# Kernel tuning notes

Hardware: AMD Instinct MI355X
Metric: run time of the kernel (lower is better)

Reference implementation:

```python
import jax, jax.numpy as jnp
import numpy as np

FP8_MAX = 448.0  # max finite value of float8_e4m3fn


def quantize_tensorwise(x):
    """Tensorwise fp8 quantization: returns fp8 tensor and inverse scale."""
    amax = jnp.max(jnp.abs(x))
    inv_scale = jnp.maximum(amax, jnp.asarray(1e-12, x.dtype)) / FP8_MAX
    q = (x / inv_scale).astype(jnp.float8_e4m3fn)
    return q, inv_scale


def setup_inputs() -> dict:
    key = jax.random.key(0)
    k1, k2, k3 = jax.random.split(key, 3)
    x = jax.random.normal(k1, (4, 1024, 4096), dtype=jnp.float32)
    weight = jax.random.normal(k2, (4096, 4096), dtype=jnp.float32) * 0.02
    bias = jax.random.normal(k3, (4096,), dtype=jnp.float32)
    return {"x": x, "weight": weight, "bias": bias}


def reference(x, weight, bias):
    out_shape = (*x.shape[:-1], weight.shape[0])
    xm = x.reshape(-1, x.shape[-1])                    # [M, K]
    fp8_x, x_inv_scale = quantize_tensorwise(xm)       # fp8 input + tensorwise scale
    fp8_wt, w_inv_scale = quantize_tensorwise(weight.T)  # weight.t() quantized, [K, N]
    # fp8 GEMM with inline dequant: (fp8_x @ fp8_w.T) * sx * sw + bias
    acc = jnp.matmul(fp8_x.astype(jnp.float32), fp8_wt.astype(jnp.float32))
    out = acc * (x_inv_scale * w_inv_scale) + bias.astype(jnp.float32)
    return out.reshape(out_shape).astype(x.dtype)
```

## Files before the change

### kernel.cpp

```cpp
#include <hip/hip_runtime.h>
#include <hip/hip_bf16.h>
#include <stdint.h>

static constexpr int M = 4096, N = 4096, K = 4096;
static constexpr float FP8_MAX = 448.0f;

using f32x16 = __attribute__((ext_vector_type(16))) float;
using i32x4  = __attribute__((ext_vector_type(4))) int;
using i32x8  = __attribute__((ext_vector_type(8))) int;

static constexpr size_t AQ_OFF   = 0;
static constexpr size_t BQ_OFF   = (size_t)M * K;
static constexpr size_t AMAX_OFF = BQ_OFF + (size_t)N * K;

__global__ __launch_bounds__(256) void amax_kernel(const float* __restrict__ x,
                                                   const float* __restrict__ w,
                                                   float* __restrict__ amax,
                                                   int n4_per_tensor,
                                                   int blocks_per_tensor) {
    const int tensor = blockIdx.x / blocks_per_tensor;
    const int blk    = blockIdx.x % blocks_per_tensor;
    const float4* src = (const float4*)(tensor == 0 ? x : w);

    float m = 0.0f;
    for (int i = blk * blockDim.x + threadIdx.x; i < n4_per_tensor;
         i += blocks_per_tensor * blockDim.x) {
        float4 v = src[i];
        m = fmaxf(m, fmaxf(fmaxf(fabsf(v.x), fabsf(v.y)),
                           fmaxf(fabsf(v.z), fabsf(v.w))));
    }
    #pragma unroll
    for (int off = 32; off >= 1; off >>= 1)
        m = fmaxf(m, __shfl_xor(m, off, 64));

    __shared__ float sm[4];
    const int lane = threadIdx.x & 63, wid = threadIdx.x >> 6;
    if (lane == 0) sm[wid] = m;
    __syncthreads();
    if (threadIdx.x == 0) {
        m = fmaxf(fmaxf(sm[0], sm[1]), fmaxf(sm[2], sm[3]));
        atomicMax((unsigned int*)&amax[tensor], __float_as_uint(m));
    }
}

__global__ __launch_bounds__(256) void quant_kernel(const float* __restrict__ x,
                                                    const float* __restrict__ w,
                                                    unsigned char* __restrict__ aq,
                                                    unsigned char* __restrict__ bq,
                                                    const float* __restrict__ amax,
                                                    int n4_per_tensor) {
    int gid = blockIdx.x * blockDim.x + threadIdx.x;
    const int tensor = (gid >= n4_per_tensor) ? 1 : 0;
    const int i = tensor ? gid - n4_per_tensor : gid;

    const float inv = fmaxf(amax[tensor], 1e-12f) / FP8_MAX;
    const float4* src = (const float4*)(tensor == 0 ? x : w);

    float4 v = src[i];
    float q0 = v.x / inv, q1 = v.y / inv, q2 = v.z / inv, q3 = v.w / inv;
    int packed = __builtin_amdgcn_cvt_pk_fp8_f32(q0, q1, 0, false);
    packed     = __builtin_amdgcn_cvt_pk_fp8_f32(q2, q3, packed, true);

    if (tensor == 0) {
        ((int*)aq)[i] = packed;
    } else {
        const int n  = i >> 10;
        const int k0 = (i & 1023) * 4;
        const int blk = (n >> 5) * (K / 64) + (k0 >> 6);
        const int ln  = (n & 31) + 32 * ((k0 >> 5) & 1);
        ((int*)bq)[blk * 512 + ln * 8 + ((k0 >> 2) & 7)] = packed;
    }
}

static constexpr int BM = 256, BN = 256, BK = 64, DEPTH = 4, NT = K / BK;

__device__ __forceinline__ void gld_lds16(const void* g, void* l) {
    __builtin_amdgcn_global_load_lds(
        (const __attribute__((address_space(1))) void*)g,
        (__attribute__((address_space(3))) void*)l, 16, 0, 0);
}

struct BReg { i32x4 lo0, hi0, lo1, hi1; };

__global__ __launch_bounds__(512, 2) void gemm_kernel(const unsigned char* __restrict__ Aq,
                                                      const unsigned char* __restrict__ Bq,
                                                      const float* __restrict__ amax,
                                                      const float* __restrict__ bias,
                                                      float* __restrict__ out) {
    __shared__ unsigned char lds[DEPTH][BM * BK];

    const int tid  = threadIdx.x;
    const int lane = tid & 63;
    const int w    = tid >> 6;
    const int wr   = w >> 2, wc = w & 3;

    const int bid = blockIdx.x;
    const int swz = (bid & 7) * 32 + (bid >> 3);
    const int brow = (swz >> 4) * BM;
    const int bcol = (swz & 15) * BN;

    const float sx = fmaxf(amax[0], 1e-12f) / FP8_MAX;
    const float sw = fmaxf(amax[1], 1e-12f) / FP8_MAX;
    const float scale = sx * sw;

    const int r4    = lane >> 2;
    const int row0  = w * 16 + r4;
    const int chk   = ((lane & 3) ^ ((row0 >> 1) & 3)) * 16;
    const unsigned char* Abase = Aq + (size_t)brow * K;

    const int frow = lane & 31;
    const int swzr = (frow >> 1) & 3;
    const int c0   = (lane >> 5) * 2;
    const int off0 = ((c0 ^ swzr) << 4);
    const int off1 = (((c0 + 1) ^ swzr) << 4);

    const unsigned char* Bf0 =
        Bq + (size_t)((bcol >> 5) + wc * 2 + 0) * (K / 64) * 2048 + (size_t)lane * 32;
    const unsigned char* Bf1 =
        Bq + (size_t)((bcol >> 5) + wc * 2 + 1) * (K / 64) * 2048 + (size_t)lane * 32;

    f32x16 acc[4][2] = {};

#define STAGE_A(t, d)                                                                          \
    do {                                                                                       \
        const size_t _k0 = (size_t)(t) * BK;                                                   \
        gld_lds16(Abase + (size_t)row0 * K + _k0 + chk,         &lds[d][w * 1024]);            \
        gld_lds16(Abase + (size_t)(row0 + 128) * K + _k0 + chk, &lds[d][8192 + w * 1024]);     \
    } while (0)

#define GLOAD_B(t, BR)                                                         \
    do {                                                                       \
        const size_t _o = (size_t)(t) * 2048;                                  \
        BR.lo0 = *(const i32x4*)(Bf0 + _o);                                    \
        BR.hi0 = *(const i32x4*)(Bf0 + _o + 16);                               \
        BR.lo1 = *(const i32x4*)(Bf1 + _o);                                    \
        BR.hi1 = *(const i32x4*)(Bf1 + _o + 16);                               \
    } while (0)

#define ITER(t, rs, ss, BRcur, BRld)                                           \
    do {                                                                       \
        asm volatile("s_waitcnt vmcnt(12)" ::: "memory");                      \
        __builtin_amdgcn_s_barrier();                                          \
        __builtin_amdgcn_sched_barrier(0);                                     \
        STAGE_A(((t) + 3 < NT) ? (t) + 3 : NT - 1, ss);                        \
        GLOAD_B(((t) + 2 < NT) ? (t) + 2 : NT - 1, BRld);                      \
        i32x8 _aF[4];                                                          \
        _Pragma("unroll")                                                      \
        for (int _mt = 0; _mt < 4; ++_mt) {                                    \
            const unsigned char* _p = &lds[rs][(wr * 128 + _mt * 32 + frow) * BK]; \
            i32x4 _lo = *(const i32x4*)(_p + off0);                            \
            i32x4 _hi = *(const i32x4*)(_p + off1);                            \
            _aF[_mt] = __builtin_shufflevector(_lo, _hi, 0, 1, 2, 3, 4, 5, 6, 7); \
        }                                                                      \
        i32x8 _b0 = __builtin_shufflevector(BRcur.lo0, BRcur.hi0, 0, 1, 2, 3, 4, 5, 6, 7); \
        i32x8 _b1 = __builtin_shufflevector(BRcur.lo1, BRcur.hi1, 0, 1, 2, 3, 4, 5, 6, 7); \
        __builtin_amdgcn_s_setprio(1);                                         \
        _Pragma("unroll")                                                      \
        for (int _mt = 0; _mt < 4; ++_mt) {                                    \
            acc[_mt][0] = __builtin_amdgcn_mfma_scale_f32_32x32x64_f8f6f4(     \
                _aF[_mt], _b0, acc[_mt][0], 0, 0, 0, 0x7F, 0, 0x7F);           \
            acc[_mt][1] = __builtin_amdgcn_mfma_scale_f32_32x32x64_f8f6f4(     \
                _aF[_mt], _b1, acc[_mt][1], 0, 0, 0, 0x7F, 0, 0x7F);           \
        }                                                                      \
        __builtin_amdgcn_s_setprio(0);                                         \
        asm volatile("s_waitcnt lgkmcnt(0)" ::: "memory");                     \
        __builtin_amdgcn_sched_barrier(0);                                     \
    } while (0)

    BReg br0, br1, br2, br3;

    STAGE_A(0, 0);
    GLOAD_B(0, br0);
    STAGE_A(1, 1);
    GLOAD_B(1, br1);
    STAGE_A(2, 2);
    asm volatile("s_waitcnt vmcnt(0)" ::: "memory");
    __builtin_amdgcn_s_barrier();
    __builtin_amdgcn_sched_barrier(0);

    for (int t = 0; t < NT; t += 4) {
        ITER(t + 0, 0, 3, br0, br2);
        ITER(t + 1, 1, 0, br1, br3);
        ITER(t + 2, 2, 1, br2, br0);
        ITER(t + 3, 3, 2, br3, br1);
    }
#undef ITER
#undef GLOAD_B
#undef STAGE_A

    #pragma unroll
    for (int mt = 0; mt < 4; ++mt) {
        const int rbase = brow + wr * 128 + mt * 32 + 4 * (lane >> 5);
        #pragma unroll
        for (int nt2 = 0; nt2 < 2; ++nt2) {
            const int col = bcol + wc * 64 + nt2 * 32 + (lane & 31);
            const float b = bias[col];
            #pragma unroll
            for (int reg = 0; reg < 16; ++reg) {
                const int row = rbase + (reg & 3) + 8 * (reg >> 2);
                out[(size_t)row * N + col] = acc[mt][nt2][reg] * scale + b;
            }
        }
    }
}

extern "C" void kernel_launch(void* const* d_in, const int* in_sizes, int n_in,
                              void* d_out, int out_size, void* d_ws, size_t ws_size,
                              hipStream_t stream) {
    const float* x    = (const float*)d_in[0];
    const float* w    = (const float*)d_in[1];
    const float* bias = (const float*)d_in[2];
    float* out = (float*)d_out;

    unsigned char* aq = (unsigned char*)d_ws + AQ_OFF;
    unsigned char* bq = (unsigned char*)d_ws + BQ_OFF;
    float* amax = (float*)((unsigned char*)d_ws + AMAX_OFF);

    const int n4 = (M * K) / 4;

    hipMemsetAsync(amax, 0, 2 * sizeof(float), stream);

    const int blocks_per_tensor = 512;
    amax_kernel<<<2 * blocks_per_tensor, 256, 0, stream>>>(x, w, amax, n4, blocks_per_tensor);

    const int quant_blocks = (2 * n4) / 256;
    quant_kernel<<<quant_blocks, 256, 0, stream>>>(x, w, aq, bq, amax, n4);

    gemm_kernel<<<256, 512, 0, stream>>>(aq, bq, amax, bias, out);
}
```

Before: 138.2 us.

## Halve GEMM M-tile to 128 and restructure B prefetch to double-buffer

```diff
diff --git a/kernel.cpp b/kernel.cpp
--- a/kernel.cpp
+++ b/kernel.cpp
@@ -72,7 +72,7 @@
     }
 }
 
-static constexpr int BM = 256, BN = 256, BK = 64, DEPTH = 4, NT = K / BK;
+static constexpr int BM = 128, BN = 256, BK = 64, DEPTH = 4, NT = K / BK;
 
 __device__ __forceinline__ void gld_lds16(const void* g, void* l) {
     __builtin_amdgcn_global_load_lds(
@@ -80,9 +80,9 @@
         (__attribute__((address_space(3))) void*)l, 16, 0, 0);
 }
 
-struct BReg { i32x4 lo0, hi0, lo1, hi1; };
-
-__global__ __launch_bounds__(512, 2) void gemm_kernel(const unsigned char* __restrict__ Aq,
+struct BPair { i32x8 b0, b1; };
+
+__global__ __launch_bounds__(512, 4) void gemm_kernel(const unsigned char* __restrict__ Aq,
                                                       const unsigned char* __restrict__ Bq,
                                                       const float* __restrict__ amax,
                                                       const float* __restrict__ bias,
@@ -95,7 +95,7 @@
     const int wr   = w >> 2, wc = w & 3;
 
     const int bid = blockIdx.x;
-    const int swz = (bid & 7) * 32 + (bid >> 3);
+    const int swz = (bid & 7) * 64 + (bid >> 3);
     const int brow = (swz >> 4) * BM;
     const int bcol = (swz & 15) * BN;
 
@@ -103,9 +103,8 @@
     const float sw = fmaxf(amax[1], 1e-12f) / FP8_MAX;
     const float scale = sx * sw;
 
-    const int r4    = lane >> 2;
-    const int row0  = w * 16 + r4;
-    const int chk   = ((lane & 3) ^ ((row0 >> 1) & 3)) * 16;
+    const int row0  = tid >> 2;
+    const int chk   = ((tid & 3) ^ ((row0 >> 1) & 3)) * 16;
     const unsigned char* Abase = Aq + (size_t)brow * K;
 
     const int frow = lane & 31;
@@ -119,78 +118,76 @@
     const unsigned char* Bf1 =
         Bq + (size_t)((bcol >> 5) + wc * 2 + 1) * (K / 64) * 2048 + (size_t)lane * 32;
 
-    f32x16 acc[4][2] = {};
-
-#define STAGE_A(t, d)                                                                          \
-    do {                                                                                       \
-        const size_t _k0 = (size_t)(t) * BK;                                                   \
-        gld_lds16(Abase + (size_t)row0 * K + _k0 + chk,         &lds[d][w * 1024]);            \
-        gld_lds16(Abase + (size_t)(row0 + 128) * K + _k0 + chk, &lds[d][8192 + w * 1024]);     \
-    } while (0)
+    f32x16 acc[2][2] = {};
+
+#define STAGE_A(t, d)                                                          \
+    gld_lds16(Abase + (size_t)row0 * K + (size_t)(t) * BK + chk,               \
+              &lds[d][(tid >> 6) * 1024])
 
 #define GLOAD_B(t, BR)                                                         \
     do {                                                                       \
         const size_t _o = (size_t)(t) * 2048;                                  \
-        BR.lo0 = *(const i32x4*)(Bf0 + _o);                                    \
-        BR.hi0 = *(const i32x4*)(Bf0 + _o + 16);                               \
-        BR.lo1 = *(const i32x4*)(Bf1 + _o);                                    \
-        BR.hi1 = *(const i32x4*)(Bf1 + _o + 16);                               \
+        BR.b0 = *(const i32x8*)(Bf0 + _o);                                     \
+        BR.b1 = *(const i32x8*)(Bf1 + _o);                                     \
     } while (0)
 
-#define ITER(t, rs, ss, BRcur, BRld)                                           \
+#define ITER(t, rs, ss, BCUR, BNXT)                                            \
     do {                                                                       \
-        asm volatile("s_waitcnt vmcnt(12)" ::: "memory");                      \
+        asm volatile("s_waitcnt vmcnt(1)" ::: "memory");                       \
         __builtin_amdgcn_s_barrier();                                          \
         __builtin_amdgcn_sched_barrier(0);                                     \
+        GLOAD_B(((t) + 1 < NT) ? (t) + 1 : NT - 1, BNXT);                      \
         STAGE_A(((t) + 3 < NT) ? (t) + 3 : NT - 1, ss);                        \
-        GLOAD_B(((t) + 2 < NT) ? (t) + 2 : NT - 1, BRld);                      \
-        i32x8 _aF[4];                                                          \
-        _Pragma("unroll")                                                      \
-        for (int _mt = 0; _mt < 4; ++_mt) {                                    \
-            const unsigned char* _p = &lds[rs][(wr * 128 + _mt * 32 + frow) * BK]; \
+        i32x8 _a0, _a1;                                                        \
+        {                                                                      \
+            const unsigned char* _p = &lds[rs][(wr * 64 + frow) * BK];         \
             i32x4 _lo = *(const i32x4*)(_p + off0);                            \
             i32x4 _hi = *(const i32x4*)(_p + off1);                            \
-            _aF[_mt] = __builtin_shufflevector(_lo, _hi, 0, 1, 2, 3, 4, 5, 6, 7); \
+            _a0 = __builtin_shufflevector(_lo, _hi, 0, 1, 2, 3, 4, 5, 6, 7);   \
         }                                                                      \
-        i32x8 _b0 = __builtin_shufflevector(BRcur.lo0, BRcur.hi0, 0, 1, 2, 3, 4, 5, 6, 7); \
-        i32x8 _b1 = __builtin_shufflevector(BRcur.lo1, BRcur.hi1, 0, 1, 2, 3, 4, 5, 6, 7); \
+        {                                                                      \
+            const unsigned char* _p = &lds[rs][(wr * 64 + 32 + frow) * BK];    \
+            i32x4 _lo = *(const i32x4*)(_p + off0);                            \
+            i32x4 _hi = *(const i32x4*)(_p + off1);                            \
+            _a1 = __builtin_shufflevector(_lo, _hi, 0, 1, 2, 3, 4, 5, 6, 7);   \
+        }                                                                      \
         __builtin_amdgcn_s_setprio(1);                                         \
-        _Pragma("unroll")                                                      \
-        for (int _mt = 0; _mt < 4; ++_mt) {                                    \
-            acc[_mt][0] = __builtin_amdgcn_mfma_scale_f32_32x32x64_f8f6f4(     \
-                _aF[_mt], _b0, acc[_mt][0], 0, 0, 0, 0x7F, 0, 0x7F);           \
-            acc[_mt][1] = __builtin_amdgcn_mfma_scale_f32_32x32x64_f8f6f4(     \
-                _aF[_mt], _b1, acc[_mt][1], 0, 0, 0, 0x7F, 0, 0x7F);           \
-        }                                                                      \
+        acc[0][0] = __builtin_amdgcn_mfma_scale_f32_32x32x64_f8f6f4(           \
+            _a0, BCUR.b0, acc[0][0], 0, 0, 0, 0x7F, 0, 0x7F);                  \
+        acc[0][1] = __builtin_amdgcn_mfma_scale_f32_32x32x64_f8f6f4(           \
+            _a0, BCUR.b1, acc[0][1], 0, 0, 0, 0x7F, 0, 0x7F);                  \
+        acc[1][0] = __builtin_amdgcn_mfma_scale_f32_32x32x64_f8f6f4(           \
+            _a1, BCUR.b0, acc[1][0], 0, 0, 0, 0x7F, 0, 0x7F);                  \
+        acc[1][1] = __builtin_amdgcn_mfma_scale_f32_32x32x64_f8f6f4(           \
+            _a1, BCUR.b1, acc[1][1], 0, 0, 0, 0x7F, 0, 0x7F);                  \
         __builtin_amdgcn_s_setprio(0);                                         \
         asm volatile("s_waitcnt lgkmcnt(0)" ::: "memory");                     \
         __builtin_amdgcn_sched_barrier(0);                                     \
     } while (0)
 
-    BReg br0, br1, br2, br3;
+    BPair bP, bQ;
 
     STAGE_A(0, 0);
-    GLOAD_B(0, br0);
     STAGE_A(1, 1);
-    GLOAD_B(1, br1);
     STAGE_A(2, 2);
+    GLOAD_B(0, bP);
     asm volatile("s_waitcnt vmcnt(0)" ::: "memory");
     __builtin_amdgcn_s_barrier();
     __builtin_amdgcn_sched_barrier(0);
 
     for (int t = 0; t < NT; t += 4) {
-        ITER(t + 0, 0, 3, br0, br2);
-        ITER(t + 1, 1, 0, br1, br3);
-        ITER(t + 2, 2, 1, br2, br0);
-        ITER(t + 3, 3, 2, br3, br1);
+        ITER(t + 0, 0, 3, bP, bQ);
+        ITER(t + 1, 1, 0, bQ, bP);
+        ITER(t + 2, 2, 1, bP, bQ);
+        ITER(t + 3, 3, 2, bQ, bP);
     }
 #undef ITER
 #undef GLOAD_B
 #undef STAGE_A
 
     #pragma unroll
-    for (int mt = 0; mt < 4; ++mt) {
-        const int rbase = brow + wr * 128 + mt * 32 + 4 * (lane >> 5);
+    for (int mt = 0; mt < 2; ++mt) {
+        const int rbase = brow + wr * 64 + mt * 32 + 4 * (lane >> 5);
         #pragma unroll
         for (int nt2 = 0; nt2 < 2; ++nt2) {
             const int col = bcol + wc * 64 + nt2 * 32 + (lane & 31);
@@ -226,5 +223,5 @@
     const int quant_blocks = (2 * n4) / 256;
     quant_kernel<<<quant_blocks, 256, 0, stream>>>(x, w, aq, bq, amax, n4);
 
-    gemm_kernel<<<256, 512, 0, stream>>>(aq, bq, amax, bias, out);
-}
+    gemm_kernel<<<512, 512, 0, stream>>>(aq, bq, amax, bias, out);
+}
```

Result: slower. 143.0 us (+3.5%).
